# Kernel optimization log

Hardware: AMD Instinct MI355X
Metric: run time of the kernel (lower is better)

The kernel has to match this reference:

```python
import jax, jax.numpy as jnp
import numpy as np

B, N, D_MODEL, H, BLK = 2, 2048, 1024, 16, 128
TB = N // BLK  # 16 blocks per side
NEG = -1e30


def setup_inputs() -> dict:
    key = jax.random.key(0)
    kq, kk, kv, kb = jax.random.split(key, 4)
    q = jax.random.normal(kq, (B, N, D_MODEL), jnp.float32)
    k = jax.random.normal(kk, (B, N, D_MODEL), jnp.float32)
    v = jax.random.normal(kv, (B, N, D_MODEL), jnp.float32)
    tau = jnp.float32(1.0)
    mask = jnp.ones((B, 1, N, N), jnp.int32)
    block_sparse_mask = jax.random.randint(kb, (TB, TB), 0, 2).astype(jnp.int32)
    return {"q": q, "k": k, "v": v, "tau": tau, "mask": mask,
            "block_sparse_mask": block_sparse_mask}


def reference(q, k, v, tau, mask, block_sparse_mask):
    # Equivalent closed form of the tiled online-softmax loop (dropout p=0, eval
    # mode): processed blocks accumulate exactly masked softmax(tau*QK^T/sqrt(dk))@V;
    # rows whose every block is skipped keep O=0, l=0, m=-inf.
    Bq, Nq, D = q.shape
    d_k = D // H
    qh = q.reshape(Bq, Nq, H, d_k).transpose(0, 2, 1, 3)  # (B,H,N,dk)
    kh = k.reshape(Bq, Nq, H, d_k).transpose(0, 2, 1, 3)
    vh = v.reshape(Bq, Nq, H, d_k).transpose(0, 2, 1, 3)

    S = tau * jnp.einsum('bhqd,bhkd->bhqk', qh, kh) / np.sqrt(d_k).astype(np.float32)

    # expand block-sparse pattern to token resolution (N,N)
    bs = jnp.repeat(jnp.repeat(block_sparse_mask, BLK, axis=0), BLK, axis=1)
    allowed = (mask != 0) & (bs != 0)  # (B,1,N,N), broadcasts over heads

    S_m = jnp.where(allowed, S, NEG)
    m = jnp.max(S_m, axis=-1, keepdims=True)            # (B,H,N,1)
    P = jnp.exp(S_m - m) * allowed.astype(S.dtype)      # masked exp-weights
    l = jnp.sum(P, axis=-1, keepdims=True)              # (B,H,N,1)
    Ov = jnp.einsum('bhqk,bhkd->bhqd', P, vh)
    O = Ov / jnp.where(l > 0, l, 1.0)

    has_any = jnp.any(allowed, axis=-1, keepdims=True)  # (B,1,N,1)
    m_out = jnp.where(has_any, m, -jnp.inf)
    O_out = O.transpose(0, 2, 1, 3).reshape(Bq, Nq, D)
    return O_out, l, m_out
```

## Files before the change

kernel.cpp:

```cpp
#include <hip/hip_runtime.h>
#include <hip/hip_bf16.h>

#define B_   2
#define N_   2048
#define DM_  1024
#define H_   16
#define DK_  64
#define BLK_ 128
#define TB_  16

typedef unsigned short u16;
typedef unsigned int   u32;
using bf16x8 = __attribute__((ext_vector_type(8))) __bf16;
using f32x4  = __attribute__((ext_vector_type(4))) float;

#define OPAD 68

__device__ __forceinline__ u32 pack_bf16(float a, float b) {
  __hip_bfloat162 h = __float22bfloat162_rn(make_float2(a, b));
  u32 u; __builtin_memcpy(&u, &h, 4); return u;
}
__device__ __forceinline__ bf16x8 pack8(float4 f0, float4 f1, float sc) {
  u32 w[4];
  w[0] = pack_bf16(f0.x * sc, f0.y * sc); w[1] = pack_bf16(f0.z * sc, f0.w * sc);
  w[2] = pack_bf16(f1.x * sc, f1.y * sc); w[3] = pack_bf16(f1.z * sc, f1.w * sc);
  bf16x8 r; __builtin_memcpy(&r, w, 16); return r;
}

__global__ void kv_convert(const float* __restrict__ k, const float* __restrict__ v,
                           u16* __restrict__ kimg, u16* __restrict__ vimg) {
  __shared__ u16 tile[BLK_][DK_ + 2];
  const int b = blockIdx.z, h = blockIdx.y, nb = blockIdx.x;
  const int t = threadIdx.x;
  const size_t obase = ((size_t)((b * H_ + h) * TB_ + nb)) * 8192;
  const int rr = t >> 4, cc = (t & 15) * 4;
  {
    const float* kg = k + ((size_t)(b * N_ + nb * BLK_)) * DM_ + h * DK_;
    u16* kd = kimg + obase;
#pragma unroll
    for (int i = 0; i < 8; ++i) {
      const int r = rr + i * 16;
      const float4 f = *(const float4*)(kg + (size_t)r * DM_ + cc);
      const int so = ((((cc >> 3) ^ (r & 7)) << 3) | (cc & 4));
      *(uint2*)(kd + r * 64 + so) = make_uint2(pack_bf16(f.x, f.y), pack_bf16(f.z, f.w));
    }
  }
  {
    const float* vg = v + ((size_t)(b * N_ + nb * BLK_)) * DM_ + h * DK_;
#pragma unroll
    for (int i = 0; i < 8; ++i) {
      const int r = rr + i * 16;
      const float4 f = *(const float4*)(vg + (size_t)r * DM_ + cc);
      *(u32*)(&tile[r][cc])     = pack_bf16(f.x, f.y);
      *(u32*)(&tile[r][cc + 2]) = pack_bf16(f.z, f.w);
    }
    __syncthreads();
    const int d = t & 63, n0 = (t >> 6) * 32;
    u16* og = vimg + obase + d * 128;
#pragma unroll
    for (int j = 0; j < 32; j += 8) {
      u16 tmp[8];
#pragma unroll
      for (int x = 0; x < 8; ++x) tmp[x] = tile[n0 + j + x][d];
      uint4 w; __builtin_memcpy(&w, tmp, 16);
      const int chunk = (n0 + j) >> 3;
      *(uint4*)(og + ((chunk ^ (d & 7)) << 3)) = w;
    }
  }
}

__global__ void mask_flags_kernel(const int* __restrict__ mask, const int* __restrict__ bs,
                                  int* __restrict__ flags) {
  const int blk = blockIdx.x;
  const int kb = blk % TB_, qb = (blk / TB_) % TB_, b = blk / (TB_ * TB_);
  const int t = threadIdx.x;
  const int* mg = mask + (size_t)b * N_ * N_ + (size_t)(qb * BLK_) * N_ + kb * BLK_;
  int all1 = 1, any1 = 0;
  for (int i = t; i < BLK_ * BLK_ / 4; i += 256) {
    const int r = i >> 5, c = (i & 31) * 4;
    const int4 mv = *(const int4*)(mg + (size_t)r * N_ + c);
    all1 &= (mv.x != 0) & (mv.y != 0) & (mv.z != 0) & (mv.w != 0);
    any1 |= (mv.x != 0) | (mv.y != 0) | (mv.z != 0) | (mv.w != 0);
  }
  __shared__ int sAll[4], sAny[4];
  const int wv = t >> 6;
  const int wAll = __all(all1), wAny = __any(any1);
  if ((t & 63) == 0) { sAll[wv] = wAll; sAny[wv] = wAny; }
  __syncthreads();
  if (t == 0) {
    const int A = sAll[0] & sAll[1] & sAll[2] & sAll[3];
    const int O = sAny[0] | sAny[1] | sAny[2] | sAny[3];
    int f = 0;
    if (bs[qb * TB_ + kb] != 0 && O) f = A ? 1 : 2;
    flags[blk] = f;
  }
}

#define STAGE(blk_, bi_) do {                                                        \
    const u16* ksrc_ = kpl + (size_t)(blk_) * 8192 + wave * 2048 + lane * 8;         \
    const u16* vsrc_ = vpl + (size_t)(blk_) * 8192 + wave * 2048 + lane * 8;         \
    u16* kdst_ = lds + (bi_) * 8192 + wave * 2048;                                   \
    u16* vdst_ = lds + 16384 + (bi_) * 8192 + wave * 2048;                           \
    _Pragma("unroll")                                                                \
    for (int i2_ = 0; i2_ < 4; ++i2_) {                                              \
      __builtin_amdgcn_global_load_lds(                                              \
          (const __attribute__((address_space(1))) void*)(ksrc_ + i2_ * 512),        \
          (__attribute__((address_space(3))) void*)(kdst_ + i2_ * 512), 16, 0, 0);   \
      __builtin_amdgcn_global_load_lds(                                              \
          (const __attribute__((address_space(1))) void*)(vsrc_ + i2_ * 512),        \
          (__attribute__((address_space(3))) void*)(vdst_ + i2_ * 512), 16, 0, 0);   \
    }                                                                                \
  } while (0)

__global__ __launch_bounds__(256, 2)
void attn_kernel(const float* __restrict__ q_, const u16* __restrict__ kimg,
                 const u16* __restrict__ vimg, const float* __restrict__ tau_p,
                 const int* __restrict__ mask, const int* __restrict__ flags,
                 float* __restrict__ o_out, float* __restrict__ l_out,
                 float* __restrict__ m_out) {
  __shared__ __align__(16) u16 lds[4 * 8192];
  float* Os = (float*)lds;

  const int idx = blockIdx.x;
  const int bh = idx & 31, qb128 = idx >> 5;
  const int b = bh >> 4, h = bh & 15;
  const int t = threadIdx.x;
  const int wave = t >> 6, lane = t & 63, quad = lane >> 4, col = lane & 15;

  const int* flg = flags + (b * TB_ + qb128) * TB_;
  u32 actmask = 0, mixmask = 0;
#pragma unroll
  for (int i = 0; i < TB_; ++i) {
    const int f = flg[i];
    actmask |= (f != 0) ? (1u << i) : 0u;
    mixmask |= (f == 2) ? (1u << i) : 0u;
  }

  const u16* kpl = kimg + (size_t)(b * H_ + h) * TB_ * 8192;
  const u16* vpl = vimg + (size_t)(b * H_ + h) * TB_ * 8192;

  u32 rem = actmask;
  int cur = -1;
  if (rem) { cur = (int)__builtin_ctz(rem); rem &= rem - 1; STAGE(cur, 0); }

  int qg[2];
  qg[0] = qb128 * BLK_ + wave * 32 + col;
  qg[1] = qg[0] + 16;

  const float qscale = tau_p[0] * 0.125f * 1.44269504f;
  bf16x8 bq[2][2];
#pragma unroll
  for (int nt = 0; nt < 2; ++nt) {
    const float* qr = q_ + ((size_t)(b * N_ + qg[nt])) * DM_ + h * DK_;
#pragma unroll
    for (int half = 0; half < 2; ++half) {
      const float4 f0 = *(const float4*)(qr + half * 32 + quad * 8);
      const float4 f1 = *(const float4*)(qr + half * 32 + quad * 8 + 4);
      bq[nt][half] = pack8(f0, f1, qscale);
    }
  }

  float m_run[2]  = {-INFINITY, -INFINITY};
  float m_true[2] = {-INFINITY, -INFINITY};
  float l_run[2] = {0.f, 0.f};
  f32x4 oacc[2][4];
#pragma unroll
  for (int nt = 0; nt < 2; ++nt)
#pragma unroll
    for (int mt = 0; mt < 4; ++mt) oacc[nt][mt] = (f32x4){0.f, 0.f, 0.f, 0.f};

  const int s8 = col & 7;
  const int a0o = (quad ^ s8) << 3;
  const int q2 = quad >> 1;

  int bufi = 0;
  while (cur >= 0) {
    __syncthreads();

    int nxt = -1;
    if (rem) { nxt = (int)__builtin_ctz(rem); rem &= rem - 1; STAGE(nxt, bufi ^ 1); }

    const int mix = (mixmask >> cur) & 1;
    const u16* KsB = lds + bufi * 8192;
    const u16* VtB = lds + 16384 + bufi * 8192;

    u32 pw[2][16];

#pragma unroll
    for (int nt = 0; nt < 2; ++nt) {
      f32x4 st[8];
      __builtin_amdgcn_s_setprio(1);
#pragma unroll
      for (int kt = 0; kt < 8; ++kt) {
        const u16* krow = KsB + (kt * 16 + col) * 64;
        const bf16x8 a0 = *(const bf16x8*)(krow + a0o);
        const bf16x8 a1 = *(const bf16x8*)(krow + (a0o ^ 32));
        f32x4 c = (f32x4){0.f, 0.f, 0.f, 0.f};
        c = __builtin_amdgcn_mfma_f32_16x16x32_bf16(a0, bq[nt][0], c, 0, 0, 0);
        c = __builtin_amdgcn_mfma_f32_16x16x32_bf16(a1, bq[nt][1], c, 0, 0, 0);
        st[kt] = c;
      }
      __builtin_amdgcn_s_setprio(0);
      if (mix) {
        const int* mg = mask + (size_t)b * N_ * N_ + (size_t)qg[nt] * N_ + cur * BLK_;
#pragma unroll
        for (int kt = 0; kt < 8; ++kt) {
          const int4 mv = *(const int4*)(mg + kt * 16 + quad * 4);
          if (!mv.x) st[kt][0] = -1e30f;
          if (!mv.y) st[kt][1] = -1e30f;
          if (!mv.z) st[kt][2] = -1e30f;
          if (!mv.w) st[kt][3] = -1e30f;
        }
      }
      float mx = -INFINITY;
#pragma unroll
      for (int kt = 0; kt < 8; ++kt)
        mx = fmaxf(mx, fmaxf(fmaxf(st[kt][0], st[kt][1]), fmaxf(st[kt][2], st[kt][3])));
      mx = fmaxf(mx, __shfl_xor(mx, 16, 64));
      mx = fmaxf(mx, __shfl_xor(mx, 32, 64));
      m_true[nt] = fmaxf(m_true[nt], mx);

      const float mold = m_run[nt];
      float mnew = mold;
      if (!__all(mx <= mold + 8.f)) {
        mnew = fmaxf(mold, mx);
        const float alpha = __builtin_amdgcn_exp2f(mold - mnew);
        l_run[nt] *= alpha;
#pragma unroll
        for (int mt = 0; mt < 4; ++mt)
#pragma unroll
          for (int r = 0; r < 4; ++r) oacc[nt][mt][r] *= alpha;
        m_run[nt] = mnew;
      }

      float s = 0.f;
      if (!mix) {
#pragma unroll
        for (int kt = 0; kt < 8; ++kt) {
          const float p0 = __builtin_amdgcn_exp2f(st[kt][0] - mnew);
          const float p1 = __builtin_amdgcn_exp2f(st[kt][1] - mnew);
          const float p2 = __builtin_amdgcn_exp2f(st[kt][2] - mnew);
          const float p3 = __builtin_amdgcn_exp2f(st[kt][3] - mnew);
          s += (p0 + p1) + (p2 + p3);
          pw[nt][kt * 2 + 0] = pack_bf16(p0, p1);
          pw[nt][kt * 2 + 1] = pack_bf16(p2, p3);
        }
      } else {
#pragma unroll
        for (int kt = 0; kt < 8; ++kt) {
          const float p0 = st[kt][0] <= -1e29f ? 0.f : __builtin_amdgcn_exp2f(st[kt][0] - mnew);
          const float p1 = st[kt][1] <= -1e29f ? 0.f : __builtin_amdgcn_exp2f(st[kt][1] - mnew);
          const float p2 = st[kt][2] <= -1e29f ? 0.f : __builtin_amdgcn_exp2f(st[kt][2] - mnew);
          const float p3 = st[kt][3] <= -1e29f ? 0.f : __builtin_amdgcn_exp2f(st[kt][3] - mnew);
          s += (p0 + p1) + (p2 + p3);
          pw[nt][kt * 2 + 0] = pack_bf16(p0, p1);
          pw[nt][kt * 2 + 1] = pack_bf16(p2, p3);
        }
      }
      s += __shfl_xor(s, 16, 64);
      s += __shfl_xor(s, 32, 64);
      l_run[nt] += s;
    }

#pragma unroll
    for (int ks = 0; ks < 4; ++ks) {
      bf16x8 bfrag[2];
#pragma unroll
      for (int nt = 0; nt < 2; ++nt) {
        const u32 wA0 = pw[nt][4 * ks + 0], wA1 = pw[nt][4 * ks + 1];
        const u32 wB0 = pw[nt][4 * ks + 2], wB1 = pw[nt][4 * ks + 3];
        const u32 a0 = q2 ? wB0 : wA0;
        const u32 a1 = q2 ? wB1 : wA1;
        const u32 b0 = q2 ? wA0 : wB0;
        const u32 b1 = q2 ? wA1 : wB1;
        const u32 x16_0 = __shfl_xor(a0, 16, 64);
        const u32 x16_1 = __shfl_xor(a1, 16, 64);
        const u32 x32_0 = __shfl_xor(b0, 32, 64);
        const u32 x32_1 = __shfl_xor(b1, 32, 64);
        const u32 x48_0 = __shfl_xor(b0, 48, 64);
        const u32 x48_1 = __shfl_xor(b1, 48, 64);
        u32 wv[4];
        wv[0] = (quad & 2) ? ((quad & 1) ? x16_0 : x32_0) : ((quad & 1) ? x48_0 : a0);
        wv[1] = (quad & 2) ? ((quad & 1) ? x16_1 : x32_1) : ((quad & 1) ? x48_1 : a1);
        wv[2] = (quad & 2) ? ((quad & 1) ? a0 : x48_0) : ((quad & 1) ? x32_0 : x16_0);
        wv[3] = (quad & 2) ? ((quad & 1) ? a1 : x48_1) : ((quad & 1) ? x32_1 : x16_1);
        __builtin_memcpy(&bfrag[nt], wv, 16);
      }
      __builtin_amdgcn_s_setprio(1);
#pragma unroll
      for (int mt = 0; mt < 4; ++mt) {
        const bf16x8 av =
            *(const bf16x8*)(VtB + (mt * 16 + col) * 128 + (((ks * 4 + quad) ^ s8) << 3));
        oacc[0][mt] = __builtin_amdgcn_mfma_f32_16x16x32_bf16(av, bfrag[0], oacc[0][mt], 0, 0, 0);
        oacc[1][mt] = __builtin_amdgcn_mfma_f32_16x16x32_bf16(av, bfrag[1], oacc[1][mt], 0, 0, 0);
      }
      __builtin_amdgcn_s_setprio(0);
    }

    bufi ^= 1;
    cur = nxt;
  }

  __syncthreads();
#pragma unroll
  for (int nt = 0; nt < 2; ++nt) {
    const float inv = l_run[nt] > 0.f ? 1.f / l_run[nt] : 1.f;
    const int qloc = wave * 32 + nt * 16 + col;
#pragma unroll
    for (int mt = 0; mt < 4; ++mt) {
      float4 w = make_float4(oacc[nt][mt][0] * inv, oacc[nt][mt][1] * inv,
                             oacc[nt][mt][2] * inv, oacc[nt][mt][3] * inv);
      *(float4*)(Os + qloc * OPAD + mt * 16 + quad * 4) = w;
    }
  }
  __syncthreads();
  float* ob = o_out + ((size_t)(b * N_ + qb128 * BLK_)) * DM_ + h * DK_;
#pragma unroll
  for (int j = 0; j < 8; ++j) {
    const int i = t + 256 * j;
    const int r = i >> 4, c4 = (i & 15) * 4;
    const float4 w = *(const float4*)(Os + r * OPAD + c4);
    *(float4*)(ob + (size_t)r * DM_ + c4) = w;
  }
  if (quad == 0) {
#pragma unroll
    for (int nt = 0; nt < 2; ++nt) {
      const size_t oi = (size_t)(b * H_ + h) * N_ + qg[nt];
      const float lv = l_run[nt] > 0.f
          ? l_run[nt] * __builtin_amdgcn_exp2f(m_run[nt] - m_true[nt]) : 0.f;
      l_out[oi] = lv;
      m_out[oi] = l_run[nt] > 0.f ? m_true[nt] * 0.69314718056f : -INFINITY;
    }
  }
}

extern "C" void kernel_launch(void* const* d_in, const int* in_sizes, int n_in,
                              void* d_out, int out_size, void* d_ws, size_t ws_size,
                              hipStream_t stream) {
  const float* q   = (const float*)d_in[0];
  const float* k   = (const float*)d_in[1];
  const float* v   = (const float*)d_in[2];
  const float* tau = (const float*)d_in[3];
  const int* mask  = (const int*)d_in[4];
  const int* bs    = (const int*)d_in[5];
  float* out = (float*)d_out;

  const size_t plane = (size_t)B_ * H_ * N_ * DK_;
  u16* kimg = (u16*)d_ws;
  u16* vimg = kimg + plane;
  int* flags = (int*)(vimg + plane);

  kv_convert<<<dim3(TB_, H_, B_), 256, 0, stream>>>(k, v, kimg, vimg);
  mask_flags_kernel<<<B_ * TB_ * TB_, 256, 0, stream>>>(mask, bs, flags);

  float* o_out = out;
  float* l_out = out + (size_t)B_ * N_ * DM_;
  float* m_out = l_out + (size_t)B_ * H_ * N_;
  attn_kernel<<<dim3(TB_ * 32), 256, 0, stream>>>(q, kimg, vimg, tau, mask, flags,
                                                  o_out, l_out, m_out);
}
```

Measured before the change: 171.6 us.

## Merge prepass kernels, drop K/V double buffering, route P through LDS

Result: faster. 159.1 us (-7.3%).

```diff
diff --git a/kernel.cpp b/kernel.cpp
--- a/kernel.cpp
+++ b/kernel.cpp
@@ -14,6 +14,7 @@
 using bf16x8 = __attribute__((ext_vector_type(8))) __bf16;
 using f32x4  = __attribute__((ext_vector_type(4))) float;
 
+#define PPAD 136
 #define OPAD 68
 
 __device__ __forceinline__ u32 pack_bf16(float a, float b) {
@@ -27,80 +28,81 @@
   bf16x8 r; __builtin_memcpy(&r, w, 16); return r;
 }
 
-__global__ void kv_convert(const float* __restrict__ k, const float* __restrict__ v,
-                           u16* __restrict__ kimg, u16* __restrict__ vimg) {
+__global__ void prepass_kernel(const float* __restrict__ k, const float* __restrict__ v,
+                               const int* __restrict__ mask, const int* __restrict__ bs,
+                               u16* __restrict__ kimg, u16* __restrict__ vimg,
+                               int* __restrict__ flags) {
   __shared__ u16 tile[BLK_][DK_ + 2];
-  const int b = blockIdx.z, h = blockIdx.y, nb = blockIdx.x;
+  __shared__ int sAll[4], sAny[4];
+  const int blk0 = blockIdx.x;
   const int t = threadIdx.x;
-  const size_t obase = ((size_t)((b * H_ + h) * TB_ + nb)) * 8192;
-  const int rr = t >> 4, cc = (t & 15) * 4;
-  {
-    const float* kg = k + ((size_t)(b * N_ + nb * BLK_)) * DM_ + h * DK_;
-    u16* kd = kimg + obase;
-#pragma unroll
-    for (int i = 0; i < 8; ++i) {
-      const int r = rr + i * 16;
-      const float4 f = *(const float4*)(kg + (size_t)r * DM_ + cc);
-      const int so = ((((cc >> 3) ^ (r & 7)) << 3) | (cc & 4));
-      *(uint2*)(kd + r * 64 + so) = make_uint2(pack_bf16(f.x, f.y), pack_bf16(f.z, f.w));
-    }
-  }
-  {
-    const float* vg = v + ((size_t)(b * N_ + nb * BLK_)) * DM_ + h * DK_;
-#pragma unroll
-    for (int i = 0; i < 8; ++i) {
-      const int r = rr + i * 16;
-      const float4 f = *(const float4*)(vg + (size_t)r * DM_ + cc);
-      *(u32*)(&tile[r][cc])     = pack_bf16(f.x, f.y);
-      *(u32*)(&tile[r][cc + 2]) = pack_bf16(f.z, f.w);
-    }
+  if (blk0 < 512) {
+    const int nb = blk0 & 15, h = (blk0 >> 4) & 15, b = blk0 >> 8;
+    const size_t obase = ((size_t)((b * H_ + h) * TB_ + nb)) * 8192;
+    const int rr = t >> 4, cc = (t & 15) * 4;
+    {
+      const float* kg = k + ((size_t)(b * N_ + nb * BLK_)) * DM_ + h * DK_;
+      u16* kd = kimg + obase;
+#pragma unroll
+      for (int i = 0; i < 8; ++i) {
+        const int r = rr + i * 16;
+        const float4 f = *(const float4*)(kg + (size_t)r * DM_ + cc);
+        const int so = ((((cc >> 3) ^ (r & 7)) << 3) | (cc & 4));
+        *(uint2*)(kd + r * 64 + so) = make_uint2(pack_bf16(f.x, f.y), pack_bf16(f.z, f.w));
+      }
+    }
+    {
+      const float* vg = v + ((size_t)(b * N_ + nb * BLK_)) * DM_ + h * DK_;
+#pragma unroll
+      for (int i = 0; i < 8; ++i) {
+        const int r = rr + i * 16;
+        const float4 f = *(const float4*)(vg + (size_t)r * DM_ + cc);
+        *(u32*)(&tile[r][cc])     = pack_bf16(f.x, f.y);
+        *(u32*)(&tile[r][cc + 2]) = pack_bf16(f.z, f.w);
+      }
+      __syncthreads();
+      const int d = t & 63, n0 = (t >> 6) * 32;
+      u16* og = vimg + obase + d * 128;
+#pragma unroll
+      for (int j = 0; j < 32; j += 8) {
+        u16 tmp[8];
+#pragma unroll
+        for (int x = 0; x < 8; ++x) tmp[x] = tile[n0 + j + x][d];
+        uint4 w; __builtin_memcpy(&w, tmp, 16);
+        const int chunk = (n0 + j) >> 3;
+        *(uint4*)(og + ((chunk ^ (d & 7)) << 3)) = w;
+      }
+    }
+  } else {
+    const int blk = blk0 - 512;
+    const int kb = blk % TB_, qb = (blk / TB_) % TB_, b = blk / (TB_ * TB_);
+    const int* mg = mask + (size_t)b * N_ * N_ + (size_t)(qb * BLK_) * N_ + kb * BLK_;
+    int all1 = 1, any1 = 0;
+    for (int i = t; i < BLK_ * BLK_ / 4; i += 256) {
+      const int r = i >> 5, c = (i & 31) * 4;
+      const int4 mv = *(const int4*)(mg + (size_t)r * N_ + c);
+      all1 &= (mv.x != 0) & (mv.y != 0) & (mv.z != 0) & (mv.w != 0);
+      any1 |= (mv.x != 0) | (mv.y != 0) | (mv.z != 0) | (mv.w != 0);
+    }
+    const int wv = t >> 6;
+    const int wAll = __all(all1), wAny = __any(any1);
+    if ((t & 63) == 0) { sAll[wv] = wAll; sAny[wv] = wAny; }
     __syncthreads();
-    const int d = t & 63, n0 = (t >> 6) * 32;
-    u16* og = vimg + obase + d * 128;
-#pragma unroll
-    for (int j = 0; j < 32; j += 8) {
-      u16 tmp[8];
-#pragma unroll
-      for (int x = 0; x < 8; ++x) tmp[x] = tile[n0 + j + x][d];
-      uint4 w; __builtin_memcpy(&w, tmp, 16);
-      const int chunk = (n0 + j) >> 3;
-      *(uint4*)(og + ((chunk ^ (d & 7)) << 3)) = w;
-    }
-  }
-}
-
-__global__ void mask_flags_kernel(const int* __restrict__ mask, const int* __restrict__ bs,
-                                  int* __restrict__ flags) {
-  const int blk = blockIdx.x;
-  const int kb = blk % TB_, qb = (blk / TB_) % TB_, b = blk / (TB_ * TB_);
-  const int t = threadIdx.x;
-  const int* mg = mask + (size_t)b * N_ * N_ + (size_t)(qb * BLK_) * N_ + kb * BLK_;
-  int all1 = 1, any1 = 0;
-  for (int i = t; i < BLK_ * BLK_ / 4; i += 256) {
-    const int r = i >> 5, c = (i & 31) * 4;
-    const int4 mv = *(const int4*)(mg + (size_t)r * N_ + c);
-    all1 &= (mv.x != 0) & (mv.y != 0) & (mv.z != 0) & (mv.w != 0);
-    any1 |= (mv.x != 0) | (mv.y != 0) | (mv.z != 0) | (mv.w != 0);
-  }
-  __shared__ int sAll[4], sAny[4];
-  const int wv = t >> 6;
-  const int wAll = __all(all1), wAny = __any(any1);
-  if ((t & 63) == 0) { sAll[wv] = wAll; sAny[wv] = wAny; }
-  __syncthreads();
-  if (t == 0) {
-    const int A = sAll[0] & sAll[1] & sAll[2] & sAll[3];
-    const int O = sAny[0] | sAny[1] | sAny[2] | sAny[3];
-    int f = 0;
-    if (bs[qb * TB_ + kb] != 0 && O) f = A ? 1 : 2;
-    flags[blk] = f;
-  }
-}
-
-#define STAGE(blk_, bi_) do {                                                        \
+    if (t == 0) {
+      const int A = sAll[0] & sAll[1] & sAll[2] & sAll[3];
+      const int O = sAny[0] | sAny[1] | sAny[2] | sAny[3];
+      int f = 0;
+      if (bs[qb * TB_ + kb] != 0 && O) f = A ? 1 : 2;
+      flags[blk] = f;
+    }
+  }
+}
+
+#define STAGE(blk_) do {                                                             \
     const u16* ksrc_ = kpl + (size_t)(blk_) * 8192 + wave * 2048 + lane * 8;         \
     const u16* vsrc_ = vpl + (size_t)(blk_) * 8192 + wave * 2048 + lane * 8;         \
-    u16* kdst_ = lds + (bi_) * 8192 + wave * 2048;                                   \
-    u16* vdst_ = lds + 16384 + (bi_) * 8192 + wave * 2048;                           \
+    u16* kdst_ = lds + wave * 2048;                                                  \
+    u16* vdst_ = lds + 8192 + wave * 2048;                                           \
     _Pragma("unroll")                                                                \
     for (int i2_ = 0; i2_ < 4; ++i2_) {                                              \
       __builtin_amdgcn_global_load_lds(                                              \
@@ -118,7 +120,8 @@
                  const int* __restrict__ mask, const int* __restrict__ flags,
                  float* __restrict__ o_out, float* __restrict__ l_out,
                  float* __restrict__ m_out) {
-  __shared__ __align__(16) u16 lds[4 * 8192];
+  __shared__ __align__(16) u16 lds[8192 + 8192 + BLK_ * PPAD];
+  u16* Ps  = lds + 16384;
   float* Os = (float*)lds;
 
   const int idx = blockIdx.x;
@@ -139,10 +142,6 @@
   const u16* kpl = kimg + (size_t)(b * H_ + h) * TB_ * 8192;
   const u16* vpl = vimg + (size_t)(b * H_ + h) * TB_ * 8192;
 
-  u32 rem = actmask;
-  int cur = -1;
-  if (rem) { cur = (int)__builtin_ctz(rem); rem &= rem - 1; STAGE(cur, 0); }
-
   int qg[2];
   qg[0] = qb128 * BLK_ + wave * 32 + col;
   qg[1] = qg[0] + 16;
@@ -171,20 +170,16 @@
 
   const int s8 = col & 7;
   const int a0o = (quad ^ s8) << 3;
-  const int q2 = quad >> 1;
-
-  int bufi = 0;
-  while (cur >= 0) {
+
+  u32 rem = actmask;
+  while (rem) {
+    const int cur = (int)__builtin_ctz(rem);
+    rem &= rem - 1;
+    const int mix = (mixmask >> cur) & 1;
+
     __syncthreads();
-
-    int nxt = -1;
-    if (rem) { nxt = (int)__builtin_ctz(rem); rem &= rem - 1; STAGE(nxt, bufi ^ 1); }
-
-    const int mix = (mixmask >> cur) & 1;
-    const u16* KsB = lds + bufi * 8192;
-    const u16* VtB = lds + 16384 + bufi * 8192;
-
-    u32 pw[2][16];
+    STAGE(cur);
+    __syncthreads();
 
 #pragma unroll
     for (int nt = 0; nt < 2; ++nt) {
@@ -192,7 +187,7 @@
       __builtin_amdgcn_s_setprio(1);
 #pragma unroll
       for (int kt = 0; kt < 8; ++kt) {
-        const u16* krow = KsB + (kt * 16 + col) * 64;
+        const u16* krow = lds + (kt * 16 + col) * 64;
         const bf16x8 a0 = *(const bf16x8*)(krow + a0o);
         const bf16x8 a1 = *(const bf16x8*)(krow + (a0o ^ 32));
         f32x4 c = (f32x4){0.f, 0.f, 0.f, 0.f};
@@ -233,6 +228,7 @@
         m_run[nt] = mnew;
       }
 
+      const int qloc = wave * 32 + nt * 16 + col;
       float s = 0.f;
       if (!mix) {
 #pragma unroll
@@ -242,8 +238,8 @@
           const float p2 = __builtin_amdgcn_exp2f(st[kt][2] - mnew);
           const float p3 = __builtin_amdgcn_exp2f(st[kt][3] - mnew);
           s += (p0 + p1) + (p2 + p3);
-          pw[nt][kt * 2 + 0] = pack_bf16(p0, p1);
-          pw[nt][kt * 2 + 1] = pack_bf16(p2, p3);
+          *(uint2*)(Ps + qloc * PPAD + kt * 16 + quad * 4) =
+              make_uint2(pack_bf16(p0, p1), pack_bf16(p2, p3));
         }
       } else {
 #pragma unroll
@@ -253,8 +249,8 @@
           const float p2 = st[kt][2] <= -1e29f ? 0.f : __builtin_amdgcn_exp2f(st[kt][2] - mnew);
           const float p3 = st[kt][3] <= -1e29f ? 0.f : __builtin_amdgcn_exp2f(st[kt][3] - mnew);
           s += (p0 + p1) + (p2 + p3);
-          pw[nt][kt * 2 + 0] = pack_bf16(p0, p1);
-          pw[nt][kt * 2 + 1] = pack_bf16(p2, p3);
+          *(uint2*)(Ps + qloc * PPAD + kt * 16 + quad * 4) =
+              make_uint2(pack_bf16(p0, p1), pack_bf16(p2, p3));
         }
       }
       s += __shfl_xor(s, 16, 64);
@@ -262,43 +258,22 @@
       l_run[nt] += s;
     }
 
+    __builtin_amdgcn_s_setprio(1);
 #pragma unroll
     for (int ks = 0; ks < 4; ++ks) {
       bf16x8 bfrag[2];
 #pragma unroll
-      for (int nt = 0; nt < 2; ++nt) {
-        const u32 wA0 = pw[nt][4 * ks + 0], wA1 = pw[nt][4 * ks + 1];
-        const u32 wB0 = pw[nt][4 * ks + 2], wB1 = pw[nt][4 * ks + 3];
-        const u32 a0 = q2 ? wB0 : wA0;
-        const u32 a1 = q2 ? wB1 : wA1;
-        const u32 b0 = q2 ? wA0 : wB0;
-        const u32 b1 = q2 ? wA1 : wB1;
-        const u32 x16_0 = __shfl_xor(a0, 16, 64);
-        const u32 x16_1 = __shfl_xor(a1, 16, 64);
-        const u32 x32_0 = __shfl_xor(b0, 32, 64);
-        const u32 x32_1 = __shfl_xor(b1, 32, 64);
-        const u32 x48_0 = __shfl_xor(b0, 48, 64);
-        const u32 x48_1 = __shfl_xor(b1, 48, 64);
-        u32 wv[4];
-        wv[0] = (quad & 2) ? ((quad & 1) ? x16_0 : x32_0) : ((quad & 1) ? x48_0 : a0);
-        wv[1] = (quad & 2) ? ((quad & 1) ? x16_1 : x32_1) : ((quad & 1) ? x48_1 : a1);
-        wv[2] = (quad & 2) ? ((quad & 1) ? a0 : x48_0) : ((quad & 1) ? x32_0 : x16_0);
-        wv[3] = (quad & 2) ? ((quad & 1) ? a1 : x48_1) : ((quad & 1) ? x32_1 : x16_1);
-        __builtin_memcpy(&bfrag[nt], wv, 16);
-      }
-      __builtin_amdgcn_s_setprio(1);
+      for (int nt = 0; nt < 2; ++nt)
+        bfrag[nt] = *(const bf16x8*)(Ps + (wave * 32 + nt * 16 + col) * PPAD + ks * 32 + quad * 8);
 #pragma unroll
       for (int mt = 0; mt < 4; ++mt) {
         const bf16x8 av =
-            *(const bf16x8*)(VtB + (mt * 16 + col) * 128 + (((ks * 4 + quad) ^ s8) << 3));
+            *(const bf16x8*)(lds + 8192 + (mt * 16 + col) * 128 + (((ks * 4 + quad) ^ s8) << 3));
         oacc[0][mt] = __builtin_amdgcn_mfma_f32_16x16x32_bf16(av, bfrag[0], oacc[0][mt], 0, 0, 0);
         oacc[1][mt] = __builtin_amdgcn_mfma_f32_16x16x32_bf16(av, bfrag[1], oacc[1][mt], 0, 0, 0);
       }
-      __builtin_amdgcn_s_setprio(0);
-    }
-
-    bufi ^= 1;
-    cur = nxt;
+    }
+    __builtin_amdgcn_s_setprio(0);
   }
 
   __syncthreads();
@@ -350,8 +325,7 @@
   u16* vimg = kimg + plane;
   int* flags = (int*)(vimg + plane);
 
-  kv_convert<<<dim3(TB_, H_, B_), 256, 0, stream>>>(k, v, kimg, vimg);
-  mask_flags_kernel<<<B_ * TB_ * TB_, 256, 0, stream>>>(mask, bs, flags);
+  prepass_kernel<<<dim3(1024), 256, 0, stream>>>(k, v, mask, bs, kimg, vimg, flags);
 
   float* o_out = out;
   float* l_out = out + (size_t)B_ * N_ * DM_;
```
